# Optimization experiments

Hardware: AMD Instinct MI355X
Metric: run time of the kernel (lower is better)

Reference implementation:

```python
import jax, jax.numpy as jnp
import numpy as np

SCALE = 3.0
NB_CLASSES = 65536
SZ_EMBED = 64
N = 4096


def _l2norm(v):
    # F.normalize(p=2, dim=-1)
    return v / jnp.maximum(jnp.linalg.norm(v, axis=-1, keepdims=True), 1e-12)


def setup_inputs() -> dict:
    key = jax.random.key(0)
    k1, k2, k3 = jax.random.split(key, 3)
    X = jax.random.normal(k1, (N, SZ_EMBED), dtype=jnp.float32)
    # proxies initialized as randn/8 in the torch module
    proxies = jax.random.normal(k2, (NB_CLASSES, SZ_EMBED), dtype=jnp.float32) / 8.0
    T = jax.random.randint(k3, (N,), 0, NB_CLASSES)
    indices = jnp.arange(N)
    return {"X": X, "proxies": proxies, "indices": indices, "T": T}


def reference(X, proxies, indices, T):
    # P = scale * normalize(proxies); X = scale * normalize(X)
    P = SCALE * _l2norm(proxies)          # [C, d]
    Xs = SCALE * _l2norm(X)               # [N, d]
    # squared pairwise distance, cross block D[:N, N:] only (same math as
    # pairwise_distance(cat([X, P]))[ :N, N: ] without the (N+C)^2 matrix)
    sq_x = jnp.sum(Xs * Xs, axis=-1, keepdims=True)   # [N, 1]
    sq_p = jnp.sum(P * P, axis=-1)                    # [C]
    D = sq_x + sq_p[None, :] - 2.0 * (Xs @ P.T)       # [N, C]
    D = jnp.maximum(D, 0.0)
    # T one-hot (smoothing_const=0): loss_i = -log_softmax(-D)[i, T[i]]
    logp = jax.nn.log_softmax(-D, axis=-1)            # [N, C]
    nll = -jnp.take_along_axis(logp, T[:, None], axis=1)[:, 0]
    return jnp.mean(nll)
```

## Files before the change

kernel.cpp:

```cpp
#include <hip/hip_runtime.h>
#include <math.h>


#define NROWS 4096
#define NCLS  65536
#define DIM   64
#define CBLK  128
#define NBLK  (NCLS / CBLK)
#define RSPLIT 2
#define NCH   (CBLK / 16)
#define NPB   (NCLS / 4)

typedef __attribute__((ext_vector_type(8))) short short8;
typedef __attribute__((ext_vector_type(4))) float f32x4;

#define PRESCALE 5.0959308f

__device__ __forceinline__ short bf16rne(float f) {
    union { float f; unsigned u; } v; v.f = f;
    unsigned r = (v.u + 0x7fffu + ((v.u >> 16) & 1u)) >> 16;
    return (short)r;
}

__global__ void k_prep(const float* __restrict__ X, const float* __restrict__ P,
                       const int* __restrict__ T,
                       unsigned short* __restrict__ Pb,
                       unsigned short* __restrict__ Xb, float* __restrict__ st,
                       float* __restrict__ out) {
    int bx = blockIdx.x;
    int t  = threadIdx.x;
    if (bx < NPB) {
        int row = bx * 4 + (t >> 6);
        int d   = t & 63;
        float v  = P[row * DIM + d];
        float sq = v * v;
        #pragma unroll
        for (int off = 32; off > 0; off >>= 1) sq += __shfl_xor(sq, off);
        float sc = PRESCALE * rsqrtf(fmaxf(sq, 1e-24f));
        int idx = (row >> 4) * 1024 + (d >> 5) * 512
                + ((row & 15) + ((d >> 3) & 3) * 16) * 8 + (d & 7);
        Pb[idx] = (unsigned short)bf16rne(v * sc);
    } else {
        if (bx == NPB && t == 0) out[0] = 0.0f;
        int row  = (bx - NPB) * 4 + (t >> 6);
        int lane = t & 63;
        int tc   = T[row];
        float xv = X[row * DIM + lane];
        float pv = P[tc  * DIM + lane];
        float x2 = xv * xv, p2 = pv * pv, xp = xv * pv;
        #pragma unroll
        for (int off = 32; off > 0; off >>= 1) {
            x2 += __shfl_xor(x2, off);
            p2 += __shfl_xor(p2, off);
            xp += __shfl_xor(xp, off);
        }
        float rx = rsqrtf(fmaxf(x2, 1e-24f));
        Xb[row * DIM + lane] = (unsigned short)bf16rne(xv * (PRESCALE * rx));
        if (lane == 0)
            st[row] = 18.0f * xp * rx * rsqrtf(fmaxf(p2, 1e-24f));
    }
}

__global__ __launch_bounds__(512, 2)
void k_main(const unsigned short* __restrict__ Pbu, const unsigned short* __restrict__ Xb,
            float* __restrict__ psum) {
    __shared__ __align__(16) unsigned short plds[NCH * 2 * 512];

    int t = threadIdx.x;
    int w = t >> 6;
    int l = t & 63;
    int bx = blockIdx.x;
    int b  = bx & (NBLK - 1);
    int h  = bx >> 9;
    int lm = l & 15;
    int lk = l >> 4;

    {
        const char* src = reinterpret_cast<const char*>(Pbu)
                        + (size_t)b * 16384 + w * 1024 + l * 16;
        __builtin_amdgcn_global_load_lds(
            (const __attribute__((address_space(1))) unsigned int*)src,
            (__attribute__((address_space(3))) unsigned int*)((char*)plds + w * 1024),
            16, 0, 0);
        __builtin_amdgcn_global_load_lds(
            (const __attribute__((address_space(1))) unsigned int*)(src + 8192),
            (__attribute__((address_space(3))) unsigned int*)((char*)plds + 8192 + w * 1024),
            16, 0, 0);
    }
    __syncthreads();

    const f32x4 zero = {0.0f, 0.0f, 0.0f, 0.0f};

    const short8* xpA = reinterpret_cast<const short8*>(
        Xb + (h * 2048 + w * 16 + lm) * DIM + lk * 8);
    float* prow = psum + ((size_t)b * NROWS + h * 2048 + w * 16 + lm) * 2 + lk;
    const char* pl = (const char*)plds + l * 16;

    #pragma unroll 1
    for (int it = 0; it < 8; ++it) {
        short8 xA0 = xpA[0];
        short8 xA1 = xpA[4];
        short8 xB0 = xpA[1024];
        short8 xB1 = xpA[1028];

        float eA0 = 0.f, eA1 = 0.f, eA2 = 0.f, eA3 = 0.f;
        float eB0 = 0.f, eB1 = 0.f, eB2 = 0.f, eB3 = 0.f;
        #pragma unroll
        for (int ch = 0; ch < NCH; ++ch) {
            short8 p0 = *reinterpret_cast<const short8*>(pl + ch * 2048);
            short8 p1 = *reinterpret_cast<const short8*>(pl + ch * 2048 + 1024);
            f32x4 cA = __builtin_amdgcn_mfma_f32_16x16x32_bf16(p0, xA0, zero, 0, 0, 0);
            cA = __builtin_amdgcn_mfma_f32_16x16x32_bf16(p1, xA1, cA, 0, 0, 0);
            f32x4 cB = __builtin_amdgcn_mfma_f32_16x16x32_bf16(p0, xB0, zero, 0, 0, 0);
            cB = __builtin_amdgcn_mfma_f32_16x16x32_bf16(p1, xB1, cB, 0, 0, 0);
            eA0 += __builtin_amdgcn_exp2f(cA[0]);
            eA1 += __builtin_amdgcn_exp2f(cA[1]);
            eA2 += __builtin_amdgcn_exp2f(cA[2]);
            eA3 += __builtin_amdgcn_exp2f(cA[3]);
            eB0 += __builtin_amdgcn_exp2f(cB[0]);
            eB1 += __builtin_amdgcn_exp2f(cB[1]);
            eB2 += __builtin_amdgcn_exp2f(cB[2]);
            eB3 += __builtin_amdgcn_exp2f(cB[3]);
        }
        float sA = (eA0 + eA1) + (eA2 + eA3);
        float sB = (eB0 + eB1) + (eB2 + eB3);
        sA += __shfl_xor(sA, 32);
        sB += __shfl_xor(sB, 32);
        if (l < 32) {
            prow[0]       = sA;
            prow[128 * 2] = sB;
        }

        xpA += 2048;
        prow += 256 * 2;
    }
}

__global__ void k_rowred(const float* __restrict__ psum, const float* __restrict__ st,
                         float* __restrict__ out) {
    __shared__ float red[256];
    __shared__ float rnll[16];
    int t  = threadIdx.x;
    int j  = t >> 4;
    int ri = t & 15;
    int r  = blockIdx.x * 16 + ri;
    const float2* p2 = reinterpret_cast<const float2*>(psum) + r;
    float s = 0.0f;
    #pragma unroll 4
    for (int i = j * 32; i < j * 32 + 32; ++i) {
        float2 v = p2[(size_t)i * NROWS];
        s += v.x + v.y;
    }
    red[t] = s;
    __syncthreads();
    if (t < 128) red[t] += red[t + 128];
    __syncthreads();
    if (t < 64)  red[t] += red[t + 64];
    __syncthreads();
    if (t < 32)  red[t] += red[t + 32];
    __syncthreads();
    if (t < 16) {
        float tot = red[t] + red[t + 16];
        rnll[t] = logf(tot) - st[r];
    }
    __syncthreads();
    if (t == 0) {
        float a = 0.0f;
        #pragma unroll
        for (int k = 0; k < 16; ++k) a += rnll[k];
        atomicAdd(out, a * (1.0f / (float)NROWS));
    }
}

extern "C" void kernel_launch(void* const* d_in, const int* in_sizes, int n_in,
                              void* d_out, int out_size, void* d_ws, size_t ws_size,
                              hipStream_t stream) {
    const float* X = (const float*)d_in[0];
    const float* P = (const float*)d_in[1];
    const int*   T = (const int*)  d_in[3];
    float* out = (float*)d_out;

    char* ws = (char*)d_ws;
    unsigned short* Xb = (unsigned short*)ws;
    float* st   = (float*)(ws + (512 << 10));
    unsigned short* Pb = (unsigned short*)(ws + (576 << 10));
    float* psum = (float*)(ws + (9 << 20));

    k_prep  <<<NPB + NROWS / 4, 256, 0, stream>>>(X, P, T, Pb, Xb, st, out);
    k_main  <<<NBLK * RSPLIT, 512, 0, stream>>>(Pb, Xb, psum);
    k_rowred<<<256, 256, 0, stream>>>(psum, st, out);
}
```

Before: 64.43 us.

## Switch main GEMM to 32x32x16 MFMA with matching proxy layout

```diff
diff --git a/kernel.cpp b/kernel.cpp
--- a/kernel.cpp
+++ b/kernel.cpp
@@ -8,11 +8,11 @@
 #define CBLK  128
 #define NBLK  (NCLS / CBLK)
 #define RSPLIT 2
-#define NCH   (CBLK / 16)
+#define NCH   (CBLK / 32)
 #define NPB   (NCLS / 4)
 
-typedef __attribute__((ext_vector_type(8))) short short8;
-typedef __attribute__((ext_vector_type(4))) float f32x4;
+typedef __attribute__((ext_vector_type(8)))  short short8;
+typedef __attribute__((ext_vector_type(16))) float f32x16;
 
 #define PRESCALE 5.0959308f
 
@@ -37,8 +37,8 @@
         #pragma unroll
         for (int off = 32; off > 0; off >>= 1) sq += __shfl_xor(sq, off);
         float sc = PRESCALE * rsqrtf(fmaxf(sq, 1e-24f));
-        int idx = (row >> 4) * 1024 + (d >> 5) * 512
-                + ((row & 15) + ((d >> 3) & 3) * 16) * 8 + (d & 7);
+        int idx = (row >> 5) * 2048 + (d >> 4) * 512
+                + ((row & 31) + 32 * ((d >> 3) & 1)) * 8 + (d & 7);
         Pb[idx] = (unsigned short)bf16rne(v * sc);
     } else {
         if (bx == NPB && t == 0) out[0] = 0.0f;
@@ -64,7 +64,7 @@
 __global__ __launch_bounds__(512, 2)
 void k_main(const unsigned short* __restrict__ Pbu, const unsigned short* __restrict__ Xb,
             float* __restrict__ psum) {
-    __shared__ __align__(16) unsigned short plds[NCH * 2 * 512];
+    __shared__ __align__(16) unsigned short plds[NCH * 2048];
 
     int t = threadIdx.x;
     int w = t >> 6;
@@ -72,8 +72,8 @@
     int bx = blockIdx.x;
     int b  = bx & (NBLK - 1);
     int h  = bx >> 9;
-    int lm = l & 15;
-    int lk = l >> 4;
+    int lc = l & 31;
+    int lk = l >> 5;
 
     {
         const char* src = reinterpret_cast<const char*>(Pbu)
@@ -89,50 +89,70 @@
     }
     __syncthreads();
 
-    const f32x4 zero = {0.0f, 0.0f, 0.0f, 0.0f};
-
-    const short8* xpA = reinterpret_cast<const short8*>(
-        Xb + (h * 2048 + w * 16 + lm) * DIM + lk * 8);
-    float* prow = psum + ((size_t)b * NROWS + h * 2048 + w * 16 + lm) * 2 + lk;
-    const char* pl = (const char*)plds + l * 16;
+    const f32x16 zero = {0.0f, 0.0f, 0.0f, 0.0f, 0.0f, 0.0f, 0.0f, 0.0f,
+                         0.0f, 0.0f, 0.0f, 0.0f, 0.0f, 0.0f, 0.0f, 0.0f};
+
+    const unsigned short* xb = Xb + (size_t)(h * 2048 + w * 32 + lc) * DIM + lk * 8;
+    float* prow = psum + (size_t)b * NROWS + h * 2048 + w * 32 + lc;
+    const char* plbase = (const char*)plds + l * 16;
 
     #pragma unroll 1
-    for (int it = 0; it < 8; ++it) {
-        short8 xA0 = xpA[0];
-        short8 xA1 = xpA[4];
-        short8 xB0 = xpA[1024];
-        short8 xB1 = xpA[1028];
+    for (int it = 0; it < 4; ++it) {
+        short8 xA0 = *reinterpret_cast<const short8*>(xb);
+        short8 xA1 = *reinterpret_cast<const short8*>(xb + 16);
+        short8 xA2 = *reinterpret_cast<const short8*>(xb + 32);
+        short8 xA3 = *reinterpret_cast<const short8*>(xb + 48);
+        short8 xB0 = *reinterpret_cast<const short8*>(xb + 16384);
+        short8 xB1 = *reinterpret_cast<const short8*>(xb + 16384 + 16);
+        short8 xB2 = *reinterpret_cast<const short8*>(xb + 16384 + 32);
+        short8 xB3 = *reinterpret_cast<const short8*>(xb + 16384 + 48);
 
         float eA0 = 0.f, eA1 = 0.f, eA2 = 0.f, eA3 = 0.f;
         float eB0 = 0.f, eB1 = 0.f, eB2 = 0.f, eB3 = 0.f;
         #pragma unroll
-        for (int ch = 0; ch < NCH; ++ch) {
-            short8 p0 = *reinterpret_cast<const short8*>(pl + ch * 2048);
-            short8 p1 = *reinterpret_cast<const short8*>(pl + ch * 2048 + 1024);
-            f32x4 cA = __builtin_amdgcn_mfma_f32_16x16x32_bf16(p0, xA0, zero, 0, 0, 0);
-            cA = __builtin_amdgcn_mfma_f32_16x16x32_bf16(p1, xA1, cA, 0, 0, 0);
-            f32x4 cB = __builtin_amdgcn_mfma_f32_16x16x32_bf16(p0, xB0, zero, 0, 0, 0);
-            cB = __builtin_amdgcn_mfma_f32_16x16x32_bf16(p1, xB1, cB, 0, 0, 0);
-            eA0 += __builtin_amdgcn_exp2f(cA[0]);
-            eA1 += __builtin_amdgcn_exp2f(cA[1]);
-            eA2 += __builtin_amdgcn_exp2f(cA[2]);
-            eA3 += __builtin_amdgcn_exp2f(cA[3]);
-            eB0 += __builtin_amdgcn_exp2f(cB[0]);
-            eB1 += __builtin_amdgcn_exp2f(cB[1]);
-            eB2 += __builtin_amdgcn_exp2f(cB[2]);
-            eB3 += __builtin_amdgcn_exp2f(cB[3]);
+        for (int cc = 0; cc < NCH; ++cc) {
+            const char* pc = plbase + cc * 4096;
+            short8 p0 = *reinterpret_cast<const short8*>(pc);
+            short8 p1 = *reinterpret_cast<const short8*>(pc + 1024);
+            short8 p2 = *reinterpret_cast<const short8*>(pc + 2048);
+            short8 p3 = *reinterpret_cast<const short8*>(pc + 3072);
+
+            f32x16 cA = __builtin_amdgcn_mfma_f32_32x32x16_bf16(p0, xA0, zero, 0, 0, 0);
+            cA = __builtin_amdgcn_mfma_f32_32x32x16_bf16(p1, xA1, cA, 0, 0, 0);
+            cA = __builtin_amdgcn_mfma_f32_32x32x16_bf16(p2, xA2, cA, 0, 0, 0);
+            cA = __builtin_amdgcn_mfma_f32_32x32x16_bf16(p3, xA3, cA, 0, 0, 0);
+            f32x16 cB = __builtin_amdgcn_mfma_f32_32x32x16_bf16(p0, xB0, zero, 0, 0, 0);
+            cB = __builtin_amdgcn_mfma_f32_32x32x16_bf16(p1, xB1, cB, 0, 0, 0);
+            cB = __builtin_amdgcn_mfma_f32_32x32x16_bf16(p2, xB2, cB, 0, 0, 0);
+            cB = __builtin_amdgcn_mfma_f32_32x32x16_bf16(p3, xB3, cB, 0, 0, 0);
+
+            #pragma unroll
+            for (int j = 0; j < 4; ++j) {
+                float a = __builtin_amdgcn_exp2f(cA[j])
+                        + __builtin_amdgcn_exp2f(cA[j + 4])
+                        + __builtin_amdgcn_exp2f(cA[j + 8])
+                        + __builtin_amdgcn_exp2f(cA[j + 12]);
+                float bb = __builtin_amdgcn_exp2f(cB[j])
+                         + __builtin_amdgcn_exp2f(cB[j + 4])
+                         + __builtin_amdgcn_exp2f(cB[j + 8])
+                         + __builtin_amdgcn_exp2f(cB[j + 12]);
+                if (j == 0)      { eA0 += a; eB0 += bb; }
+                else if (j == 1) { eA1 += a; eB1 += bb; }
+                else if (j == 2) { eA2 += a; eB2 += bb; }
+                else             { eA3 += a; eB3 += bb; }
+            }
         }
         float sA = (eA0 + eA1) + (eA2 + eA3);
         float sB = (eB0 + eB1) + (eB2 + eB3);
         sA += __shfl_xor(sA, 32);
         sB += __shfl_xor(sB, 32);
         if (l < 32) {
-            prow[0]       = sA;
-            prow[128 * 2] = sB;
+            prow[0]   = sA;
+            prow[256] = sB;
         }
 
-        xpA += 2048;
-        prow += 256 * 2;
+        xb   += 512 * DIM;
+        prow += 512;
     }
 }
 
@@ -144,13 +164,10 @@
     int j  = t >> 4;
     int ri = t & 15;
     int r  = blockIdx.x * 16 + ri;
-    const float2* p2 = reinterpret_cast<const float2*>(psum) + r;
     float s = 0.0f;
     #pragma unroll 4
-    for (int i = j * 32; i < j * 32 + 32; ++i) {
-        float2 v = p2[(size_t)i * NROWS];
-        s += v.x + v.y;
-    }
+    for (int i = j * 32; i < j * 32 + 32; ++i)
+        s += psum[(size_t)i * NROWS + r];
     red[t] = s;
     __syncthreads();
     if (t < 128) red[t] += red[t + 128];
```

After: 70.26 us. 1.09x slower.
